# Kernel optimization log

Hardware: AMD Instinct MI355X
Metric: run time of the kernel (lower is better)

Reference implementation:

```python
import jax, jax.numpy as jnp
import numpy as np

VOCAB = 100000
D = 128
B = 256
L = 2048  # leaves per tree (power of two -> complete binary tree)


def setup_inputs() -> dict:
    key = jax.random.key(0)
    k1, k2, k3, k4 = jax.random.split(key, 4)
    word_ids = jax.random.randint(k1, (B, L), 0, VOCAB)
    embedding = jax.random.normal(k2, (VOCAB, D), dtype=jnp.float32) * 0.1
    # torch nn.Linear(2*D, D): weight [D, 2*D], bias [D]
    W = jax.random.normal(k3, (D, 2 * D), dtype=jnp.float32) * (1.0 / np.sqrt(2 * D))
    b = jax.random.normal(k4, (D,), dtype=jnp.float32) * 0.01
    return {"word_ids": word_ids, "embedding": embedding, "W": W, "b": b}


def reference(word_ids, embedding, W, b):
    # Leaves: embedding lookup for every leaf of every tree. [B, L, D]
    x = embedding[word_ids]
    # Internal nodes, batched by depth: each level combines adjacent pairs
    # via linear(concat(left, right)). log2(L) levels (static unroll).
    while x.shape[1] > 1:
        left = x[:, 0::2, :]   # [B, n/2, D]
        right = x[:, 1::2, :]  # [B, n/2, D]
        pair = jnp.concatenate([left, right], axis=-1)  # [B, n/2, 2D]
        x = jnp.einsum('bnd,od->bno', pair, W) + b      # [B, n/2, D]
    return x[:, 0, :]  # root result per tree, [B, D]
```

## Files before the change

kernel.cpp:

```cpp
#include <hip/hip_runtime.h>


typedef __bf16 bf16x8 __attribute__((ext_vector_type(8)));
typedef __bf16 bf16x4 __attribute__((ext_vector_type(4)));
typedef float f32x4 __attribute__((ext_vector_type(4)));
typedef float f32x8 __attribute__((ext_vector_type(8)));

#define STRIDE 136

__global__ __launch_bounds__(256) void prep_kernel(
    const float* __restrict__ W, const float* __restrict__ emb,
    __bf16* __restrict__ wpack, __bf16* __restrict__ ebf)
{
    const int tid = threadIdx.x;
    const int blk = blockIdx.x;
    if (blk < 16) {
        const int f = blk;
        const int wv = tid >> 6, l = tid & 63;
        const int nl = f >> 3, kk = f & 7;
        const int o = ((wv << 1) + nl) * 16 + (l & 15);
        const int d = kk * 32 + ((l >> 4) << 3);
        const float* src = W + o * 256 + d;
        bf16x8 h;
#pragma unroll
        for (int j = 0; j < 8; ++j) h[j] = (__bf16)src[j];
        *(bf16x8*)(wpack + (size_t)(f * 256 + tid) * 8) = h;
    } else {
        const size_t base = ((size_t)(blk - 16) * 256 + tid) * 8;
        const f32x8 v = *(const f32x8*)(emb + base);
        *(bf16x8*)(ebf + base) = __builtin_convertvector(v, bf16x8);
    }
}

__global__ void pack_w_kernel(const float* __restrict__ W,
                              __bf16* __restrict__ wpack) {
    const int f = blockIdx.x;
    const int tid = threadIdx.x;
    const int wv = tid >> 6, l = tid & 63;
    const int nl = f >> 3, kk = f & 7;
    const int o = ((wv << 1) + nl) * 16 + (l & 15);
    const int d = kk * 32 + ((l >> 4) << 3);
    const float* src = W + o * 256 + d;
    bf16x8 h;
#pragma unroll
    for (int j = 0; j < 8; ++j) h[j] = (__bf16)src[j];
    *(bf16x8*)(wpack + (size_t)(f * 256 + tid) * 8) = h;
}

__device__ __forceinline__ void tree64_levels(
    __bf16 (*buf)[64 * STRIDE], const bf16x8* wf, const float* bval,
    int wv, int q, int lm, __bf16* yrow)
{
    int nin = 64, rb = 0;
    while (nin > 1) {
        const int nout = nin >> 1;
        const int ntm = (nout + 15) >> 4;
        for (int mt = 0; mt < ntm; ++mt) {
            const int m = mt * 16 + lm;
            bf16x8 af[8];
#pragma unroll
            for (int kk = 0; kk < 8; ++kk) {
                const int k = kk * 32 + q * 8;
                const int row = 2 * m + (k >> 7);
                const int col = k & 127;
                af[kk] = *(const bf16x8*)&buf[rb][row * STRIDE + col];
            }
#pragma unroll
            for (int nl = 0; nl < 2; ++nl) {
                f32x4 acc = { bval[nl], bval[nl], bval[nl], bval[nl] };
#pragma unroll
                for (int kk = 0; kk < 8; ++kk)
                    acc = __builtin_amdgcn_mfma_f32_16x16x32_bf16(
                        af[kk], wf[nl * 8 + kk], acc, 0, 0, 0);
                const int col = (2 * wv + nl) * 16 + lm;
                if (nout == 1) {
                    if (q == 0) yrow[col] = (__bf16)acc[0];
                } else {
                    const bf16x4 hv = __builtin_convertvector(acc, bf16x4);
#pragma unroll
                    for (int r = 0; r < 4; ++r) {
                        const int row = mt * 16 + q * 4 + r;
                        if (row < nout)
                            buf[rb ^ 1][row * STRIDE + col] = hv[r];
                    }
                }
            }
        }
        __syncthreads();
        rb ^= 1;
        nin = nout;
    }
}

__global__ __launch_bounds__(256) void tree64_kernel(
    const int* __restrict__ wid, const __bf16* __restrict__ ebf,
    const __bf16* __restrict__ wpack, const float* __restrict__ bias,
    __bf16* __restrict__ yout)
{
    __shared__ __align__(16) __bf16 buf[2][64 * STRIDE];
    __shared__ int ids[64];
    const int tid = threadIdx.x;
    const int batch = blockIdx.x >> 5;
    const int sub = blockIdx.x & 31;
    const int wv = tid >> 6, ln = tid & 63, q = ln >> 4, lm = ln & 15;

    if (tid < 64) ids[tid] = wid[batch * 2048 + sub * 64 + tid];

    bf16x8 wf[16];
    const bf16x8* wp = (const bf16x8*)wpack;
#pragma unroll
    for (int f = 0; f < 16; ++f) wf[f] = wp[f * 256 + tid];
    float bval[2];
    bval[0] = bias[(2 * wv + 0) * 16 + lm];
    bval[1] = bias[(2 * wv + 1) * 16 + lm];

    __syncthreads();

#pragma unroll
    for (int i = 0; i < 4; ++i) {
        const int flat = tid + 256 * i;
        const int row = flat >> 4;
        const int c8 = flat & 15;
        const bf16x8 v = *(const bf16x8*)(ebf + (size_t)ids[row] * 128 + c8 * 8);
        *(bf16x8*)&buf[0][row * STRIDE + c8 * 8] = v;
    }
    __syncthreads();

    tree64_levels(buf, wf, bval, wv, q, lm,
                  yout + (size_t)(batch * 32 + sub) * 128);
}

__global__ __launch_bounds__(256) void tree64_f32_kernel(
    const int* __restrict__ wid, const float* __restrict__ emb,
    const __bf16* __restrict__ wpack, const float* __restrict__ bias,
    __bf16* __restrict__ yout)
{
    __shared__ __align__(16) __bf16 buf[2][64 * STRIDE];
    __shared__ int ids[64];
    const int tid = threadIdx.x;
    const int batch = blockIdx.x >> 5;
    const int sub = blockIdx.x & 31;
    const int wv = tid >> 6, ln = tid & 63, q = ln >> 4, lm = ln & 15;

    if (tid < 64) ids[tid] = wid[batch * 2048 + sub * 64 + tid];

    bf16x8 wf[16];
    const bf16x8* wp = (const bf16x8*)wpack;
#pragma unroll
    for (int f = 0; f < 16; ++f) wf[f] = wp[f * 256 + tid];
    float bval[2];
    bval[0] = bias[(2 * wv + 0) * 16 + lm];
    bval[1] = bias[(2 * wv + 1) * 16 + lm];

    __syncthreads();

#pragma unroll
    for (int i = 0; i < 8; ++i) {
        const int flat = tid + 256 * i;
        const int row = flat >> 5;
        const int c4 = flat & 31;
        const f32x4 v = *(const f32x4*)(emb + (size_t)ids[row] * 128 + c4 * 4);
        *(bf16x4*)&buf[0][row * STRIDE + c4 * 4] =
            __builtin_convertvector(v, bf16x4);
    }
    __syncthreads();

    tree64_levels(buf, wf, bval, wv, q, lm,
                  yout + (size_t)(batch * 32 + sub) * 128);
}

__global__ __launch_bounds__(256) void tree32_kernel(
    const __bf16* __restrict__ yin, const __bf16* __restrict__ wpack,
    const float* __restrict__ bias, float* __restrict__ out)
{
    __shared__ __align__(16) __bf16 buf[2][32 * STRIDE];
    const int tid = threadIdx.x;
    const int batch = blockIdx.x;
    const int wv = tid >> 6, ln = tid & 63, q = ln >> 4, lm = ln & 15;

    bf16x8 wf[16];
    const bf16x8* wp = (const bf16x8*)wpack;
#pragma unroll
    for (int f = 0; f < 16; ++f) wf[f] = wp[f * 256 + tid];
    float bval[2];
    bval[0] = bias[(2 * wv + 0) * 16 + lm];
    bval[1] = bias[(2 * wv + 1) * 16 + lm];

#pragma unroll
    for (int i = 0; i < 2; ++i) {
        const int flat = tid + 256 * i;
        const int row = flat >> 4;
        const int c8 = flat & 15;
        const bf16x8 v =
            *(const bf16x8*)(yin + (size_t)(batch * 32 + row) * 128 + c8 * 8);
        *(bf16x8*)&buf[0][row * STRIDE + c8 * 8] = v;
    }
    __syncthreads();

    int nin = 32, rb = 0;
    while (nin > 1) {
        const int nout = nin >> 1;
        const int m = lm;
        bf16x8 af[8];
#pragma unroll
        for (int kk = 0; kk < 8; ++kk) {
            const int k = kk * 32 + q * 8;
            const int row = 2 * m + (k >> 7);
            const int col = k & 127;
            af[kk] = *(const bf16x8*)&buf[rb][row * STRIDE + col];
        }
#pragma unroll
        for (int nl = 0; nl < 2; ++nl) {
            f32x4 acc = { bval[nl], bval[nl], bval[nl], bval[nl] };
#pragma unroll
            for (int kk = 0; kk < 8; ++kk)
                acc = __builtin_amdgcn_mfma_f32_16x16x32_bf16(
                    af[kk], wf[nl * 8 + kk], acc, 0, 0, 0);
            const int col = (2 * wv + nl) * 16 + lm;
            if (nout == 1) {
                if (q == 0) out[(size_t)batch * 128 + col] = acc[0];
            } else {
                const bf16x4 hv = __builtin_convertvector(acc, bf16x4);
#pragma unroll
                for (int r = 0; r < 4; ++r) {
                    const int row = q * 4 + r;
                    if (row < nout)
                        buf[rb ^ 1][row * STRIDE + col] = hv[r];
                }
            }
        }
        __syncthreads();
        rb ^= 1;
        nin = nout;
    }
}

extern "C" void kernel_launch(void* const* d_in, const int* in_sizes, int n_in,
                              void* d_out, int out_size, void* d_ws, size_t ws_size,
                              hipStream_t stream) {
    const int*   wid = (const int*)d_in[0];
    const float* emb = (const float*)d_in[1];
    const float* W   = (const float*)d_in[2];
    const float* b   = (const float*)d_in[3];
    float* out = (float*)d_out;

    __bf16* wpack = (__bf16*)d_ws;
    __bf16* ebf   = wpack + 32768;
    __bf16* y     = ebf + 12800000;
    const size_t need = (32768 + 12800000 + 256 * 32 * 128) * sizeof(__bf16);

    if (ws_size >= need) {
        prep_kernel<<<16 + 6250, 256, 0, stream>>>(W, emb, wpack, ebf);
        tree64_kernel<<<8192, 256, 0, stream>>>(wid, ebf, wpack, b, y);
        tree32_kernel<<<256, 256, 0, stream>>>(y, wpack, b, out);
    } else {
        __bf16* y2 = wpack + 32768;
        pack_w_kernel<<<16, 256, 0, stream>>>(W, wpack);
        tree64_f32_kernel<<<8192, 256, 0, stream>>>(wid, emb, wpack, b, y2);
        tree32_kernel<<<256, 256, 0, stream>>>(y2, wpack, b, out);
    }
}
```

Before: 146.7 us.

## Process 128-leaf subtrees per block, halving blocks and weight reloads

Result: faster. 139.1 us (-5.2%).

```diff
diff --git a/kernel.cpp b/kernel.cpp
--- a/kernel.cpp
+++ b/kernel.cpp
@@ -47,23 +47,26 @@
     *(bf16x8*)(wpack + (size_t)(f * 256 + tid) * 8) = h;
 }
 
-__device__ __forceinline__ void tree64_levels(
-    __bf16 (*buf)[64 * STRIDE], const bf16x8* wf, const float* bval,
+__device__ __forceinline__ void tree128_levels(
+    __bf16* bufA, __bf16* bufB, const bf16x8* wf, const float* bval,
     int wv, int q, int lm, __bf16* yrow)
 {
-    int nin = 64, rb = 0;
-    while (nin > 1) {
+    int nin = 128, rb = 0;
+    while (nin > 2) {
         const int nout = nin >> 1;
+        const __bf16* src = rb ? bufB : bufA;
+        __bf16* dst = rb ? bufA : bufB;
         const int ntm = (nout + 15) >> 4;
         for (int mt = 0; mt < ntm; ++mt) {
             const int m = mt * 16 + lm;
+            const int me = (m < nout) ? m : 0;
             bf16x8 af[8];
 #pragma unroll
             for (int kk = 0; kk < 8; ++kk) {
                 const int k = kk * 32 + q * 8;
-                const int row = 2 * m + (k >> 7);
+                const int row = 2 * me + (k >> 7);
                 const int col = k & 127;
-                af[kk] = *(const bf16x8*)&buf[rb][row * STRIDE + col];
+                af[kk] = *(const bf16x8*)&src[row * STRIDE + col];
             }
 #pragma unroll
             for (int nl = 0; nl < 2; ++nl) {
@@ -73,15 +76,18 @@
                     acc = __builtin_amdgcn_mfma_f32_16x16x32_bf16(
                         af[kk], wf[nl * 8 + kk], acc, 0, 0, 0);
                 const int col = (2 * wv + nl) * 16 + lm;
-                if (nout == 1) {
-                    if (q == 0) yrow[col] = (__bf16)acc[0];
+                if (nout == 2) {
+                    if (q == 0) {
+                        yrow[0 * 128 + col] = (__bf16)acc[0];
+                        yrow[1 * 128 + col] = (__bf16)acc[1];
+                    }
                 } else {
                     const bf16x4 hv = __builtin_convertvector(acc, bf16x4);
 #pragma unroll
                     for (int r = 0; r < 4; ++r) {
                         const int row = mt * 16 + q * 4 + r;
                         if (row < nout)
-                            buf[rb ^ 1][row * STRIDE + col] = hv[r];
+                            dst[row * STRIDE + col] = hv[r];
                     }
                 }
             }
@@ -92,19 +98,20 @@
     }
 }
 
-__global__ __launch_bounds__(256) void tree64_kernel(
+__global__ __launch_bounds__(256) void tree128_kernel(
     const int* __restrict__ wid, const __bf16* __restrict__ ebf,
     const __bf16* __restrict__ wpack, const float* __restrict__ bias,
     __bf16* __restrict__ yout)
 {
-    __shared__ __align__(16) __bf16 buf[2][64 * STRIDE];
-    __shared__ int ids[64];
-    const int tid = threadIdx.x;
-    const int batch = blockIdx.x >> 5;
-    const int sub = blockIdx.x & 31;
+    __shared__ __align__(16) __bf16 bufA[128 * STRIDE];
+    __shared__ __align__(16) __bf16 bufB[64 * STRIDE];
+    __shared__ int ids[128];
+    const int tid = threadIdx.x;
+    const int batch = blockIdx.x >> 4;
+    const int grp = blockIdx.x & 15;
     const int wv = tid >> 6, ln = tid & 63, q = ln >> 4, lm = ln & 15;
 
-    if (tid < 64) ids[tid] = wid[batch * 2048 + sub * 64 + tid];
+    if (tid < 128) ids[tid] = wid[batch * 2048 + grp * 128 + tid];
 
     bf16x8 wf[16];
     const bf16x8* wp = (const bf16x8*)wpack;
@@ -117,32 +124,33 @@
     __syncthreads();
 
 #pragma unroll
-    for (int i = 0; i < 4; ++i) {
+    for (int i = 0; i < 8; ++i) {
         const int flat = tid + 256 * i;
         const int row = flat >> 4;
         const int c8 = flat & 15;
         const bf16x8 v = *(const bf16x8*)(ebf + (size_t)ids[row] * 128 + c8 * 8);
-        *(bf16x8*)&buf[0][row * STRIDE + c8 * 8] = v;
-    }
-    __syncthreads();
-
-    tree64_levels(buf, wf, bval, wv, q, lm,
-                  yout + (size_t)(batch * 32 + sub) * 128);
-}
-
-__global__ __launch_bounds__(256) void tree64_f32_kernel(
+        *(bf16x8*)&bufA[row * STRIDE + c8 * 8] = v;
+    }
+    __syncthreads();
+
+    tree128_levels(bufA, bufB, wf, bval, wv, q, lm,
+                   yout + (size_t)(batch * 32 + grp * 2) * 128);
+}
+
+__global__ __launch_bounds__(256) void tree128_f32_kernel(
     const int* __restrict__ wid, const float* __restrict__ emb,
     const __bf16* __restrict__ wpack, const float* __restrict__ bias,
     __bf16* __restrict__ yout)
 {
-    __shared__ __align__(16) __bf16 buf[2][64 * STRIDE];
-    __shared__ int ids[64];
-    const int tid = threadIdx.x;
-    const int batch = blockIdx.x >> 5;
-    const int sub = blockIdx.x & 31;
+    __shared__ __align__(16) __bf16 bufA[128 * STRIDE];
+    __shared__ __align__(16) __bf16 bufB[64 * STRIDE];
+    __shared__ int ids[128];
+    const int tid = threadIdx.x;
+    const int batch = blockIdx.x >> 4;
+    const int grp = blockIdx.x & 15;
     const int wv = tid >> 6, ln = tid & 63, q = ln >> 4, lm = ln & 15;
 
-    if (tid < 64) ids[tid] = wid[batch * 2048 + sub * 64 + tid];
+    if (tid < 128) ids[tid] = wid[batch * 2048 + grp * 128 + tid];
 
     bf16x8 wf[16];
     const bf16x8* wp = (const bf16x8*)wpack;
@@ -155,18 +163,18 @@
     __syncthreads();
 
 #pragma unroll
-    for (int i = 0; i < 8; ++i) {
+    for (int i = 0; i < 16; ++i) {
         const int flat = tid + 256 * i;
         const int row = flat >> 5;
         const int c4 = flat & 31;
         const f32x4 v = *(const f32x4*)(emb + (size_t)ids[row] * 128 + c4 * 4);
-        *(bf16x4*)&buf[0][row * STRIDE + c4 * 4] =
+        *(bf16x4*)&bufA[row * STRIDE + c4 * 4] =
             __builtin_convertvector(v, bf16x4);
     }
     __syncthreads();
 
-    tree64_levels(buf, wf, bval, wv, q, lm,
-                  yout + (size_t)(batch * 32 + sub) * 128);
+    tree128_levels(bufA, bufB, wf, bval, wv, q, lm,
+                   yout + (size_t)(batch * 32 + grp * 2) * 128);
 }
 
 __global__ __launch_bounds__(256) void tree32_kernel(
@@ -201,11 +209,12 @@
     while (nin > 1) {
         const int nout = nin >> 1;
         const int m = lm;
+        const int me = (m < nout) ? m : 0;
         bf16x8 af[8];
 #pragma unroll
         for (int kk = 0; kk < 8; ++kk) {
             const int k = kk * 32 + q * 8;
-            const int row = 2 * m + (k >> 7);
+            const int row = 2 * me + (k >> 7);
             const int col = k & 127;
             af[kk] = *(const bf16x8*)&buf[rb][row * STRIDE + col];
         }
@@ -251,12 +260,12 @@
 
     if (ws_size >= need) {
         prep_kernel<<<16 + 6250, 256, 0, stream>>>(W, emb, wpack, ebf);
-        tree64_kernel<<<8192, 256, 0, stream>>>(wid, ebf, wpack, b, y);
+        tree128_kernel<<<4096, 256, 0, stream>>>(wid, ebf, wpack, b, y);
         tree32_kernel<<<256, 256, 0, stream>>>(y, wpack, b, out);
     } else {
         __bf16* y2 = wpack + 32768;
         pack_w_kernel<<<16, 256, 0, stream>>>(W, wpack);
-        tree64_f32_kernel<<<8192, 256, 0, stream>>>(wid, emb, wpack, b, y2);
+        tree128_f32_kernel<<<4096, 256, 0, stream>>>(wid, emb, wpack, b, y2);
         tree32_kernel<<<256, 256, 0, stream>>>(y2, wpack, b, out);
     }
 }
```
